# Kernel tuning notes

Hardware: AMD Instinct MI355X
Metric: run time of the kernel (lower is better)

## Reference

```python
import jax, jax.numpy as jnp
import numpy as np

BATCH = 128
SEQ_CTX = 64          # seq_len - 1 context steps
INPUT_SIZE = 320
OUTPUT_SIZE = 64
ITEM_DIM = INPUT_SIZE - OUTPUT_SIZE   # 256
HIDDEN = 1024
ONE_HOT = 192
BETA = 1.0


def setup_inputs() -> dict:
    key = jax.random.key(0)
    ks = jax.random.split(key, 6)
    return {
        "x_c": jax.random.normal(ks[0], (BATCH, SEQ_CTX, INPUT_SIZE), dtype=jnp.float32),
        "x_q": jax.random.normal(ks[1], (BATCH, ITEM_DIM), dtype=jnp.float32),
        "context_input": jax.random.uniform(ks[2], (BATCH, SEQ_CTX, ONE_HOT), dtype=jnp.float32),
        # W_hi initialized uniform(0, 0.5) as in the torch module
        "W_hi": jax.random.uniform(ks[3], (BATCH, HIDDEN, ITEM_DIM), dtype=jnp.float32) * 0.5,
        "W_oh": jax.random.uniform(ks[4], (BATCH, OUTPUT_SIZE, HIDDEN), dtype=jnp.float32),
        "W_reinst": jax.random.uniform(ks[5], (BATCH, HIDDEN, ONE_HOT), dtype=jnp.float32),
    }


def _context_scan(x_c, context_input, W_hi, W_oh, W_reinst):
    """Sequential one-winner Hebbian updates over the context sequence."""
    def step(carry, xs):
        W_hi, W_oh, W_reinst = carry
        x_curr, ctx = xs                              # (B, INPUT_SIZE), (B, ONE_HOT)
        x_item = x_curr[:, :ITEM_DIM]                 # (B, ITEM_DIM)
        x_label = x_curr[:, ITEM_DIM:]                # (B, OUTPUT_SIZE)
        logits = jnp.einsum('bhd,bd->bh', W_hi, x_item)
        # winner-take-all: one-hot of top-1 hidden unit (sparsify_tensor, k=1)
        z = jax.nn.one_hot(jnp.argmax(logits, axis=1), HIDDEN, dtype=W_hi.dtype)
        zc = z[:, :, None]                            # (B, H, 1)
        # W += z (x - W) : winner row overwritten with current pattern
        W_reinst = W_reinst + zc * (ctx[:, None, :] - W_reinst)
        W_hi = W_hi + zc * (x_item[:, None, :] - W_hi)
        W_oh = W_oh + z[:, None, :] * (x_label[:, :, None] - W_oh)
        return (W_hi, W_oh, W_reinst), None

    xs = (jnp.moveaxis(x_c, 1, 0), jnp.moveaxis(context_input, 1, 0))
    (W_hi, W_oh, W_reinst), _ = jax.lax.scan(step, (W_hi, W_oh, W_reinst), xs)
    return W_hi, W_oh, W_reinst


def reference(x_c, x_q, context_input, W_hi, W_oh, W_reinst):
    W_hi, W_oh, W_reinst = _context_scan(x_c, context_input, W_hi, W_oh, W_reinst)
    # query step
    logits = jnp.einsum('bhd,bd->bh', W_hi, x_q)          # (B, H)
    a = jax.nn.softmax(BETA * logits, axis=1)             # (B, H)
    out = jnp.einsum('boh,bh->bo', W_oh, a)               # (B, OUTPUT_SIZE)
    reinst_context = jnp.einsum('bhc,bh->bc', W_reinst, a)  # (B, ONE_HOT)
    return out, reinst_context
```

## Files before the change

kernel.cpp:

```cpp
#include <hip/hip_runtime.h>
#include <math.h>
#include <float.h>

#define BATCH 128
#define SEQ 64
#define IN 320
#define OUT 64
#define ITEM 256
#define HID 1024
#define OH 192
#define T65 65
#define KC 32
#define LDW 36

__device__ __forceinline__ void bett(float& bv, int& bh, float v, int h) {
  if (v > bv || (v == bv && h < bh)) { bv = v; bh = h; }
}

template<int R, int WROWS>
__device__ __forceinline__ void gemm_body(
    const float* __restrict__ wbase, int wstride,
    const float* __restrict__ xcb, const float* __restrict__ xqb,
    float* __restrict__ Ws, float* __restrict__ Xs,
    int tid, int lane, float (&acc)[R][8], float (&accq)[R])
{
  const int rg = lane >> 3, cg = lane & 7;
  const int wv = tid >> 6;
  const int rowbase = wv * (8 * R);

  for (int kc = 0; kc < ITEM; kc += KC) {
    __syncthreads();
    #pragma unroll
    for (int u0 = 0; u0 < WROWS * (KC / 4); u0 += 256) {
      const int u = u0 + tid;
      const int row = u >> 3, kq = (u & 7) << 2;
      const float4 v = *reinterpret_cast<const float4*>(wbase + (size_t)row * wstride + kc + kq);
      *reinterpret_cast<float4*>(&Ws[row * LDW + kq]) = v;
    }
    #pragma unroll
    for (int u0 = 0; u0 < T65 * (KC / 4); u0 += 256) {
      const int u = u0 + tid;
      if (u < T65 * (KC / 4)) {
        const int row = u >> 3, kq = (u & 7) << 2;
        const float* src = (row < 64) ? (xcb + (size_t)row * IN) : xqb;
        const float4 v = *reinterpret_cast<const float4*>(src + kc + kq);
        *reinterpret_cast<float4*>(&Xs[row * LDW + kq]) = v;
      }
    }
    __syncthreads();

    #pragma unroll 2
    for (int ks = 0; ks < KC; ks += 4) {
      float4 wf[R];
      #pragma unroll
      for (int i = 0; i < R; ++i)
        wf[i] = *reinterpret_cast<const float4*>(&Ws[(rowbase + rg + 8 * i) * LDW + ks]);
      const float4 qf = *reinterpret_cast<const float4*>(&Xs[64 * LDW + ks]);
      #pragma unroll
      for (int j = 0; j < 8; ++j) {
        const float4 xf = *reinterpret_cast<const float4*>(&Xs[(cg + 8 * j) * LDW + ks]);
        #pragma unroll
        for (int i = 0; i < R; ++i)
          acc[i][j] = fmaf(wf[i].w, xf.w, fmaf(wf[i].z, xf.z,
                      fmaf(wf[i].y, xf.y, fmaf(wf[i].x, xf.x, acc[i][j]))));
      }
      #pragma unroll
      for (int i = 0; i < R; ++i)
        accq[i] = fmaf(wf[i].w, qf.w, fmaf(wf[i].z, qf.z,
                  fmaf(wf[i].y, qf.y, fmaf(wf[i].x, qf.x, accq[i]))));
    }
  }
}

__global__ __launch_bounds__(256, 4) void k_gemm(
    const float* __restrict__ W_hi, const float* __restrict__ x_c,
    const float* __restrict__ x_q, float* __restrict__ G, float* __restrict__ X)
{
  const int b = blockIdx.y, tile = blockIdx.x;
  const int tid = threadIdx.x, lane = tid & 63;
  const int rg = lane >> 3, cg = lane & 7, wv = tid >> 6;
  __shared__ float Ws[256 * LDW];
  __shared__ float Xs[T65 * LDW];
  const float* xcb = x_c + (size_t)b * SEQ * IN;
  const float* xqb = x_q + (size_t)b * ITEM;

  if (tile < 4) {
    float acc[8][8] = {}; float accq[8] = {};
    gemm_body<8, 256>(W_hi + ((size_t)b * HID + tile * 256) * ITEM, ITEM,
                      xcb, xqb, Ws, Xs, tid, lane, acc, accq);
    const int hb = tile * 256 + wv * 64 + rg;
    #pragma unroll
    for (int i = 0; i < 8; ++i) {
      const int h = hb + 8 * i;
      #pragma unroll
      for (int j = 0; j < 8; ++j)
        G[((size_t)b * T65 + (cg + 8 * j)) * HID + h] = acc[i][j];
      if (cg == 0) G[((size_t)b * T65 + 64) * HID + h] = accq[i];
    }
  } else {
    float acc[2][8] = {}; float accq[2] = {};
    gemm_body<2, 64>(xcb, IN, xcb, xqb, Ws, Xs, tid, lane, acc, accq);
    const int sb = wv * 16 + rg;
    #pragma unroll
    for (int i = 0; i < 2; ++i) {
      const int s = sb + 8 * i;
      #pragma unroll
      for (int j = 0; j < 8; ++j)
        X[((size_t)b * T65 + (cg + 8 * j)) * SEQ + s] = acc[i][j];
      if (cg == 0) X[((size_t)b * T65 + 64) * SEQ + s] = accq[i];
    }
  }
}

__global__ __launch_bounds__(64) void k_scan(
    const float* __restrict__ G, const float* __restrict__ X,
    float* __restrict__ a_mod, float* __restrict__ t_a)
{
  const int b = blockIdx.x, lane = threadIdx.x;
  __shared__ float Xs[T65 * SEQ];
  {
    const float4* Xsrc = reinterpret_cast<const float4*>(X + (size_t)b * T65 * SEQ);
    float4* Xd = reinterpret_cast<float4*>(Xs);
    for (int i = lane; i < T65 * SEQ / 4; i += 64) Xd[i] = Xsrc[i];
  }
  const float* Gb = G + (size_t)b * T65 * HID;
  float g0[16], g1[16];
  #pragma unroll
  for (int i = 0; i < 16; ++i) g0[i] = Gb[lane + 64 * i];
  #pragma unroll
  for (int i = 0; i < 16; ++i) g1[i] = Gb[HID + lane + 64 * i];
  __syncthreads();

  unsigned vmask = 0xFFFFu;
  int myrow = 0x7FFFFFFF;
  bool active = false;

  for (int t = 0; t < SEQ; ++t) {
    const int tn = (t + 2 < 64) ? (t + 2) : 64;
    const float* Gn = Gb + (size_t)tn * HID;
    float g2[16];
    #pragma unroll
    for (int i = 0; i < 16; ++i) g2[i] = Gn[lane + 64 * i];

    float bv = -FLT_MAX; int bh = 0x7FFFFFFF;
    #pragma unroll
    for (int i = 0; i < 16; ++i) {
      const float v = ((vmask >> i) & 1u) ? g0[i] : -FLT_MAX;
      bett(bv, bh, v, lane + (i << 6));
    }
    {
      const float v = active ? Xs[t * SEQ + lane] : -FLT_MAX;
      bett(bv, bh, v, myrow);
    }
    #pragma unroll
    for (int m = 1; m < 64; m <<= 1) {
      const float ov = __shfl_xor(bv, m, 64);
      const int oh = __shfl_xor(bh, m, 64);
      bett(bv, bh, ov, oh);
    }
    if (active && myrow == bh) active = false;
    if (lane == t) { active = true; myrow = bh; }
    if ((bh & 63) == lane) vmask &= ~(1u << (bh >> 6));
    #pragma unroll
    for (int i = 0; i < 16; ++i) { g0[i] = g1[i]; g1[i] = g2[i]; }
  }

  float e[16];
  float mx = -FLT_MAX;
  #pragma unroll
  for (int i = 0; i < 16; ++i) {
    e[i] = ((vmask >> i) & 1u) ? g0[i] : -FLT_MAX;
    mx = fmaxf(mx, e[i]);
  }
  const float lt = active ? Xs[64 * SEQ + lane] : -FLT_MAX;
  mx = fmaxf(mx, lt);
  #pragma unroll
  for (int m = 1; m < 64; m <<= 1) mx = fmaxf(mx, __shfl_xor(mx, m, 64));
  float ssum = 0.f;
  #pragma unroll
  for (int i = 0; i < 16; ++i) {
    e[i] = ((vmask >> i) & 1u) ? expf(e[i] - mx) : 0.f;
    ssum += e[i];
  }
  const float et = active ? expf(lt - mx) : 0.f;
  ssum += et;
  #pragma unroll
  for (int m = 1; m < 64; m <<= 1) ssum += __shfl_xor(ssum, m, 64);
  const float inv = 1.f / ssum;
  #pragma unroll
  for (int i = 0; i < 16; ++i)
    a_mod[(size_t)b * HID + lane + 64 * i] = e[i] * inv;
  t_a[b * SEQ + lane] = et * inv;
}

__global__ __launch_bounds__(256) void k_partial(
    const float* __restrict__ W_oh, const float* __restrict__ W_re,
    const float* __restrict__ a_mod, float* __restrict__ p_out, float* __restrict__ p_re)
{
  const int b = blockIdx.y, p = blockIdx.x;
  const int tid = threadIdx.x;
  const int h0 = p * 256;
  __shared__ float as[256];
  as[tid] = a_mod[(size_t)b * HID + h0 + tid];
  __syncthreads();

  const int wv = tid >> 6, lane = tid & 63;
  if (wv < 3) {
    const int c = tid;
    const float* Wr = W_re + ((size_t)b * HID + h0) * OH + c;
    float acc = 0.f;
    #pragma unroll 16
    for (int h = 0; h < 256; ++h)
      acc = fmaf(Wr[(size_t)h * OH], as[h], acc);
    p_re[((size_t)b * 4 + p) * OH + c] = acc;
  } else {
    for (int o = 0; o < 64; ++o) {
      const float4 w4 = *reinterpret_cast<const float4*>(
          W_oh + ((size_t)b * OUT + o) * HID + h0 + lane * 4);
      const float* ap = &as[lane * 4];
      float acc = w4.x * ap[0] + w4.y * ap[1] + w4.z * ap[2] + w4.w * ap[3];
      #pragma unroll
      for (int m = 1; m < 64; m <<= 1) acc += __shfl_xor(acc, m, 64);
      if (lane == 0) p_out[((size_t)b * 4 + p) * OUT + o] = acc;
    }
  }
}

__global__ __launch_bounds__(256) void k_final(
    const float* __restrict__ x_c, const float* __restrict__ ctx,
    const float* __restrict__ p_out, const float* __restrict__ p_re,
    const float* __restrict__ t_a, float* __restrict__ out)
{
  const int b = blockIdx.x, tid = threadIdx.x;
  __shared__ float sa[SEQ];
  if (tid < SEQ) sa[tid] = t_a[b * SEQ + tid];
  __syncthreads();
  if (tid < OUT) {
    const int o = tid;
    float acc = 0.f;
    #pragma unroll
    for (int p = 0; p < 4; ++p) acc += p_out[((size_t)b * 4 + p) * OUT + o];
    for (int j = 0; j < SEQ; ++j) {
      const float w = sa[j];
      if (w != 0.f) acc = fmaf(x_c[((size_t)b * SEQ + j) * IN + ITEM + o], w, acc);
    }
    out[(size_t)b * OUT + o] = acc;
  } else if (tid < OUT + OH) {
    const int c = tid - OUT;
    float acc = 0.f;
    #pragma unroll
    for (int p = 0; p < 4; ++p) acc += p_re[((size_t)b * 4 + p) * OH + c];
    for (int j = 0; j < SEQ; ++j) {
      const float w = sa[j];
      if (w != 0.f) acc = fmaf(ctx[((size_t)b * SEQ + j) * OH + c], w, acc);
    }
    out[(size_t)BATCH * OUT + (size_t)b * OH + c] = acc;
  }
}

extern "C" void kernel_launch(void* const* d_in, const int* in_sizes, int n_in,
                              void* d_out, int out_size, void* d_ws, size_t ws_size,
                              hipStream_t stream)
{
  const float* x_c  = (const float*)d_in[0];
  const float* x_q  = (const float*)d_in[1];
  const float* ctx  = (const float*)d_in[2];
  const float* W_hi = (const float*)d_in[3];
  const float* W_oh = (const float*)d_in[4];
  const float* W_re = (const float*)d_in[5];

  char* ws = (char*)d_ws;
  float* G     = (float*)(ws);
  float* X     = (float*)(ws + 34078720);
  float* a_mod = (float*)(ws + 36208640);
  float* t_a   = (float*)(ws + 36732928);
  float* p_out = (float*)(ws + 36765696);
  float* p_re  = (float*)(ws + 36896768);

  k_gemm<<<dim3(5, BATCH), 256, 0, stream>>>(W_hi, x_c, x_q, G, X);
  k_scan<<<dim3(BATCH), 64, 0, stream>>>(G, X, a_mod, t_a);
  k_partial<<<dim3(4, BATCH), 256, 0, stream>>>(W_oh, W_re, a_mod, p_out, p_re);
  k_final<<<dim3(BATCH), 256, 0, stream>>>(x_c, ctx, p_out, p_re, t_a, (float*)d_out);
}
```

Measured before the change: 500.7 us.

## Halve GEMM tiles, vectorize scan loads, split partial readout into two kernels

The W_hi GEMM now uses 128-row tiles (9 blocks per batch) to give more parallelism and smaller shared memory. The scan kernel gives each lane 16 contiguous hidden units loaded as float4, rotates a three-step register prefetch, and replaces the paired value/index shuffle argmax with a max-reduce followed by a ballot. The readout is split into separate W_reinst and W_oh kernels, with the W_oh kernel reading full rows as float4 and reducing over 2 halves. The extra launches and more partials to sum in k_final add some overhead.

```diff
diff --git a/kernel.cpp b/kernel.cpp
--- a/kernel.cpp
+++ b/kernel.cpp
@@ -16,6 +16,9 @@
 __device__ __forceinline__ void bett(float& bv, int& bh, float v, int h) {
   if (v > bv || (v == bv && h < bh)) { bv = v; bh = h; }
 }
+__device__ __forceinline__ float f4c(const float4& v, int i) {
+  return i == 0 ? v.x : (i == 1 ? v.y : (i == 2 ? v.z : v.w));
+}
 
 template<int R, int WROWS>
 __device__ __forceinline__ void gemm_body(
@@ -79,18 +82,18 @@
   const int b = blockIdx.y, tile = blockIdx.x;
   const int tid = threadIdx.x, lane = tid & 63;
   const int rg = lane >> 3, cg = lane & 7, wv = tid >> 6;
-  __shared__ float Ws[256 * LDW];
+  __shared__ float Ws[128 * LDW];
   __shared__ float Xs[T65 * LDW];
   const float* xcb = x_c + (size_t)b * SEQ * IN;
   const float* xqb = x_q + (size_t)b * ITEM;
 
-  if (tile < 4) {
-    float acc[8][8] = {}; float accq[8] = {};
-    gemm_body<8, 256>(W_hi + ((size_t)b * HID + tile * 256) * ITEM, ITEM,
+  if (tile < 8) {
+    float acc[4][8] = {}; float accq[4] = {};
+    gemm_body<4, 128>(W_hi + ((size_t)b * HID + tile * 128) * ITEM, ITEM,
                       xcb, xqb, Ws, Xs, tid, lane, acc, accq);
-    const int hb = tile * 256 + wv * 64 + rg;
-    #pragma unroll
-    for (int i = 0; i < 8; ++i) {
+    const int hb = tile * 128 + wv * 32 + rg;
+    #pragma unroll
+    for (int i = 0; i < 4; ++i) {
       const int h = hb + 8 * i;
       #pragma unroll
       for (int j = 0; j < 8; ++j)
@@ -124,53 +127,61 @@
     for (int i = lane; i < T65 * SEQ / 4; i += 64) Xd[i] = Xsrc[i];
   }
   const float* Gb = G + (size_t)b * T65 * HID;
-  float g0[16], g1[16];
-  #pragma unroll
-  for (int i = 0; i < 16; ++i) g0[i] = Gb[lane + 64 * i];
-  #pragma unroll
-  for (int i = 0; i < 16; ++i) g1[i] = Gb[HID + lane + 64 * i];
+  const int hbase = lane << 4;
+
+  float4 gb0[4], gb1[4], gb2[4];
+  {
+    const float4* Gv0 = reinterpret_cast<const float4*>(Gb + 0 * HID + hbase);
+    const float4* Gv1 = reinterpret_cast<const float4*>(Gb + 1 * HID + hbase);
+    const float4* Gv2 = reinterpret_cast<const float4*>(Gb + 2 * HID + hbase);
+    #pragma unroll
+    for (int q = 0; q < 4; ++q) { gb0[q] = Gv0[q]; gb1[q] = Gv1[q]; gb2[q] = Gv2[q]; }
+  }
   __syncthreads();
 
   unsigned vmask = 0xFFFFu;
   int myrow = 0x7FFFFFFF;
   bool active = false;
 
-  for (int t = 0; t < SEQ; ++t) {
-    const int tn = (t + 2 < 64) ? (t + 2) : 64;
-    const float* Gn = Gb + (size_t)tn * HID;
-    float g2[16];
-    #pragma unroll
-    for (int i = 0; i < 16; ++i) g2[i] = Gn[lane + 64 * i];
-
+  auto step = [&](int t, float4 (&g)[4]) {
+    const float sv = active ? Xs[t * SEQ + lane] : -FLT_MAX;
     float bv = -FLT_MAX; int bh = 0x7FFFFFFF;
     #pragma unroll
-    for (int i = 0; i < 16; ++i) {
-      const float v = ((vmask >> i) & 1u) ? g0[i] : -FLT_MAX;
-      bett(bv, bh, v, lane + (i << 6));
-    }
+    for (int r = 0; r < 16; ++r) {
+      const float v = ((vmask >> r) & 1u) ? f4c(g[r >> 2], r & 3) : -FLT_MAX;
+      bett(bv, bh, v, hbase + r);
+    }
+    bett(bv, bh, sv, myrow);
     {
-      const float v = active ? Xs[t * SEQ + lane] : -FLT_MAX;
-      bett(bv, bh, v, myrow);
-    }
-    #pragma unroll
-    for (int m = 1; m < 64; m <<= 1) {
-      const float ov = __shfl_xor(bv, m, 64);
-      const int oh = __shfl_xor(bh, m, 64);
-      bett(bv, bh, ov, oh);
-    }
-    if (active && myrow == bh) active = false;
-    if (lane == t) { active = true; myrow = bh; }
-    if ((bh & 63) == lane) vmask &= ~(1u << (bh >> 6));
-    #pragma unroll
-    for (int i = 0; i < 16; ++i) { g0[i] = g1[i]; g1[i] = g2[i]; }
-  }
+      const int rown = (t + 3 < 64) ? (t + 3) : 64;
+      const float4* Gv = reinterpret_cast<const float4*>(Gb + (size_t)rown * HID + hbase);
+      #pragma unroll
+      for (int q = 0; q < 4; ++q) g[q] = Gv[q];
+    }
+    float gm = bv;
+    #pragma unroll
+    for (int m = 1; m < 64; m <<= 1) gm = fmaxf(gm, __shfl_xor(gm, m, 64));
+    const unsigned long long tied = __ballot(bv == gm);
+    const int srcl = __ffsll(tied) - 1;
+    const int winner = __shfl(bh, srcl, 64);
+    if (active && myrow == winner) active = false;
+    if (lane == t) { active = true; myrow = winner; }
+    if ((winner >> 4) == lane) vmask &= ~(1u << (winner & 15));
+  };
+
+  for (int tb = 0; tb < 63; tb += 3) {
+    step(tb + 0, gb0);
+    step(tb + 1, gb1);
+    step(tb + 2, gb2);
+  }
+  step(63, gb0);
 
   float e[16];
   float mx = -FLT_MAX;
   #pragma unroll
-  for (int i = 0; i < 16; ++i) {
-    e[i] = ((vmask >> i) & 1u) ? g0[i] : -FLT_MAX;
-    mx = fmaxf(mx, e[i]);
+  for (int r = 0; r < 16; ++r) {
+    e[r] = ((vmask >> r) & 1u) ? f4c(gb1[r >> 2], r & 3) : -FLT_MAX;
+    mx = fmaxf(mx, e[r]);
   }
   const float lt = active ? Xs[64 * SEQ + lane] : -FLT_MAX;
   mx = fmaxf(mx, lt);
@@ -178,51 +189,69 @@
   for (int m = 1; m < 64; m <<= 1) mx = fmaxf(mx, __shfl_xor(mx, m, 64));
   float ssum = 0.f;
   #pragma unroll
-  for (int i = 0; i < 16; ++i) {
-    e[i] = ((vmask >> i) & 1u) ? expf(e[i] - mx) : 0.f;
-    ssum += e[i];
+  for (int r = 0; r < 16; ++r) {
+    e[r] = ((vmask >> r) & 1u) ? expf(e[r] - mx) : 0.f;
+    ssum += e[r];
   }
   const float et = active ? expf(lt - mx) : 0.f;
   ssum += et;
   #pragma unroll
   for (int m = 1; m < 64; m <<= 1) ssum += __shfl_xor(ssum, m, 64);
   const float inv = 1.f / ssum;
-  #pragma unroll
-  for (int i = 0; i < 16; ++i)
-    a_mod[(size_t)b * HID + lane + 64 * i] = e[i] * inv;
+  float4* Ad = reinterpret_cast<float4*>(a_mod + (size_t)b * HID + hbase);
+  #pragma unroll
+  for (int q = 0; q < 4; ++q) {
+    float4 st;
+    st.x = e[4 * q + 0] * inv; st.y = e[4 * q + 1] * inv;
+    st.z = e[4 * q + 2] * inv; st.w = e[4 * q + 3] * inv;
+    Ad[q] = st;
+  }
   t_a[b * SEQ + lane] = et * inv;
 }
 
-__global__ __launch_bounds__(256) void k_partial(
-    const float* __restrict__ W_oh, const float* __restrict__ W_re,
-    const float* __restrict__ a_mod, float* __restrict__ p_out, float* __restrict__ p_re)
+__global__ __launch_bounds__(192) void k_part_re(
+    const float* __restrict__ W_re, const float* __restrict__ a_mod,
+    float* __restrict__ p_re)
 {
   const int b = blockIdx.y, p = blockIdx.x;
   const int tid = threadIdx.x;
-  const int h0 = p * 256;
-  __shared__ float as[256];
-  as[tid] = a_mod[(size_t)b * HID + h0 + tid];
+  const int h0 = p * 128;
+  __shared__ float as[128];
+  if (tid < 128) as[tid] = a_mod[(size_t)b * HID + h0 + tid];
   __syncthreads();
-
-  const int wv = tid >> 6, lane = tid & 63;
-  if (wv < 3) {
-    const int c = tid;
-    const float* Wr = W_re + ((size_t)b * HID + h0) * OH + c;
+  const int c = tid;
+  const float* Wr = W_re + ((size_t)b * HID + h0) * OH + c;
+  float acc = 0.f;
+  #pragma unroll 16
+  for (int h = 0; h < 128; ++h)
+    acc = fmaf(Wr[(size_t)h * OH], as[h], acc);
+  p_re[((size_t)b * 8 + p) * OH + c] = acc;
+}
+
+__global__ __launch_bounds__(256) void k_part_out(
+    const float* __restrict__ W_oh, const float* __restrict__ a_mod,
+    float* __restrict__ p_out)
+{
+  const int b = blockIdx.y, half = blockIdx.x;
+  const int tid = threadIdx.x, wv = tid >> 6, lane = tid & 63;
+  __shared__ float4 as4[256];
+  as4[tid] = reinterpret_cast<const float4*>(a_mod + (size_t)b * HID)[tid];
+  __syncthreads();
+  const int o0 = half * 32 + wv * 8;
+  #pragma unroll
+  for (int oi = 0; oi < 8; ++oi) {
+    const int o = o0 + oi;
+    const float4* W4 = reinterpret_cast<const float4*>(W_oh + ((size_t)b * OUT + o) * HID);
     float acc = 0.f;
-    #pragma unroll 16
-    for (int h = 0; h < 256; ++h)
-      acc = fmaf(Wr[(size_t)h * OH], as[h], acc);
-    p_re[((size_t)b * 4 + p) * OH + c] = acc;
-  } else {
-    for (int o = 0; o < 64; ++o) {
-      const float4 w4 = *reinterpret_cast<const float4*>(
-          W_oh + ((size_t)b * OUT + o) * HID + h0 + lane * 4);
-      const float* ap = &as[lane * 4];
-      float acc = w4.x * ap[0] + w4.y * ap[1] + w4.z * ap[2] + w4.w * ap[3];
-      #pragma unroll
-      for (int m = 1; m < 64; m <<= 1) acc += __shfl_xor(acc, m, 64);
-      if (lane == 0) p_out[((size_t)b * 4 + p) * OUT + o] = acc;
-    }
+    #pragma unroll
+    for (int k = 0; k < 4; ++k) {
+      const float4 w = W4[lane + 64 * k];
+      const float4 a = as4[lane + 64 * k];
+      acc += w.x * a.x + w.y * a.y + w.z * a.z + w.w * a.w;
+    }
+    #pragma unroll
+    for (int m = 1; m < 64; m <<= 1) acc += __shfl_xor(acc, m, 64);
+    if (lane == 0) p_out[((size_t)b * 2 + half) * OUT + o] = acc;
   }
 }
 
@@ -237,9 +266,7 @@
   __syncthreads();
   if (tid < OUT) {
     const int o = tid;
-    float acc = 0.f;
-    #pragma unroll
-    for (int p = 0; p < 4; ++p) acc += p_out[((size_t)b * 4 + p) * OUT + o];
+    float acc = p_out[((size_t)b * 2 + 0) * OUT + o] + p_out[((size_t)b * 2 + 1) * OUT + o];
     for (int j = 0; j < SEQ; ++j) {
       const float w = sa[j];
       if (w != 0.f) acc = fmaf(x_c[((size_t)b * SEQ + j) * IN + ITEM + o], w, acc);
@@ -249,7 +276,7 @@
     const int c = tid - OUT;
     float acc = 0.f;
     #pragma unroll
-    for (int p = 0; p < 4; ++p) acc += p_re[((size_t)b * 4 + p) * OH + c];
+    for (int p = 0; p < 8; ++p) acc += p_re[((size_t)b * 8 + p) * OH + c];
     for (int j = 0; j < SEQ; ++j) {
       const float w = sa[j];
       if (w != 0.f) acc = fmaf(ctx[((size_t)b * SEQ + j) * OH + c], w, acc);
@@ -275,10 +302,11 @@
   float* a_mod = (float*)(ws + 36208640);
   float* t_a   = (float*)(ws + 36732928);
   float* p_out = (float*)(ws + 36765696);
-  float* p_re  = (float*)(ws + 36896768);
-
-  k_gemm<<<dim3(5, BATCH), 256, 0, stream>>>(W_hi, x_c, x_q, G, X);
+  float* p_re  = (float*)(ws + 36831232);
+
+  k_gemm<<<dim3(9, BATCH), 256, 0, stream>>>(W_hi, x_c, x_q, G, X);
   k_scan<<<dim3(BATCH), 64, 0, stream>>>(G, X, a_mod, t_a);
-  k_partial<<<dim3(4, BATCH), 256, 0, stream>>>(W_oh, W_re, a_mod, p_out, p_re);
+  k_part_re<<<dim3(8, BATCH), 192, 0, stream>>>(W_re, a_mod, p_re);
+  k_part_out<<<dim3(2, BATCH), 256, 0, stream>>>(W_oh, a_mod, p_out);
   k_final<<<dim3(BATCH), 256, 0, stream>>>(x_c, ctx, p_out, p_re, t_a, (float*)d_out);
 }
```

Result: faster. 482.3 us (-3.7%).
